# Optimization experiments

Hardware: AMD Instinct MI355X
Metric: run time of the kernel (lower is better)

## Reference

```python
import jax, jax.numpy as jnp
import numpy as np

B, T, I, H, O = 64, 32, 512, 256, 512
NPRE = 25  # range(1, 26) in the source


def _lstm(xg, whh, mask, reverse):
    """xg: [B,T,4H] precomputed input-gate activations; mask: [T] bool.
    Masked steps keep the carry unchanged (carry starts at zeros, and the
    invalid region is always a contiguous run at the start of the scan
    direction, so this exactly reproduces running the LSTM on the valid
    sub-sequence only)."""
    nb = xg.shape[0]
    nh = whh.shape[1]

    def step(carry, inp):
        h, c = carry
        g, m = inp
        z = g + h @ whh.T  # [B,4H]
        i, f, gg, o = jnp.split(z, 4, axis=-1)  # torch gate order i,f,g,o
        c2 = jax.nn.sigmoid(f) * c + jax.nn.sigmoid(i) * jnp.tanh(gg)
        h2 = jax.nn.sigmoid(o) * jnp.tanh(c2)
        h2 = jnp.where(m, h2, h)
        c2 = jnp.where(m, c2, c)
        return (h2, c2), h2

    init = (jnp.zeros((nb, nh), xg.dtype), jnp.zeros((nb, nh), xg.dtype))
    xs = (jnp.swapaxes(xg, 0, 1), mask[:, None, None])  # time-major
    _, hs = jax.lax.scan(step, init, xs, reverse=reverse)
    return jnp.swapaxes(hs, 0, 1)  # [B,T,H]


def _bilstm(x, mask, wif, whf, bf, wib, whb, bb):
    xgf = jnp.einsum('bti,gi->btg', x, wif) + bf
    xgb = jnp.einsum('bti,gi->btg', x, wib) + bb
    hf = _lstm(xgf, whf, mask, reverse=False)
    hb = _lstm(xgb, whb, mask, reverse=True)
    return jnp.concatenate([hf, hb], axis=-1)  # [B,T,2H]


def setup_inputs() -> dict:
    key = jax.random.key(0)
    ks = jax.random.split(key, 16)
    s = 1.0 / np.sqrt(H)
    u = lambda k, shp: jax.random.uniform(k, shp, jnp.float32, -s, s)
    return {
        'x': jax.random.normal(ks[0], (B, T, I), jnp.float32),
        'w_ih_f': u(ks[1], (4 * H, I)), 'w_hh_f': u(ks[2], (4 * H, H)), 'b_f': u(ks[3], (4 * H,)),
        'w_ih_b': u(ks[4], (4 * H, I)), 'w_hh_b': u(ks[5], (4 * H, H)), 'b_b': u(ks[6], (4 * H,)),
        'w2_ih_f': u(ks[7], (4 * H, H)), 'w2_hh_f': u(ks[8], (4 * H, H)), 'b2_f': u(ks[9], (4 * H,)),
        'w2_ih_b': u(ks[10], (4 * H, H)), 'w2_hh_b': u(ks[11], (4 * H, H)), 'b2_b': u(ks[12], (4 * H,)),
        'wl': u(ks[13], (O, 4 * H)), 'bl': u(ks[14], (O,)),
    }


def reference(x, w_ih_f, w_hh_f, b_f, w_ih_b, w_hh_b, b_b,
              w2_ih_f, w2_hh_f, b2_f, w2_ih_b, w2_hh_b, b2_b, wl, bl):
    t_idx = jnp.arange(T)
    lens = jnp.arange(1, NPRE + 1)
    pre_masks = t_idx[None, :] < lens[:, None]   # [25,T]: input[:, :i]
    suf_masks = t_idx[None, :] >= lens[:, None]  # [25,T]: input[:, j:]

    run = jax.vmap(lambda m: _bilstm(x, m, w_ih_f, w_hh_f, b_f, w_ih_b, w_hh_b, b_b))
    pre = run(pre_masks)  # [25,B,T,2H]
    suf = run(suf_masks)  # [25,B,T,2H]

    neg = jnp.finfo(x.dtype).min
    prefix_pool = jnp.where(pre_masks[:, None, :, None], pre, neg).max(axis=2)  # [25,B,2H]
    suffix_pool = jnp.where(suf_masks[:, None, :, None], suf, neg).max(axis=2)  # [25,B,2H]

    full = jnp.ones((T,), bool)
    r2 = _bilstm(x[:, :, :H], full, w2_ih_f, w2_hh_f, b2_f, w2_ih_b, w2_hh_b, b2_b)
    r3 = _bilstm(x[:, :, H:], full, w2_ih_f, w2_hh_f, b2_f, w2_ih_b, w2_hh_b, b2_b)
    r4 = jnp.concatenate([r2, r3], axis=-1)  # [B,T,4H]
    output = r4 @ wl.T + bl  # [B,T,O]
    return output, prefix_pool, suffix_pool
```

## Files before the change

### kernel.cpp

```cpp
#include <hip/hip_runtime.h>
#include <math.h>

#define BB 64
#define TT 32
#define II 512
#define HH 256
#define ZN 1024
#define OO 512
#define NPRE 25

typedef unsigned short u16;
typedef unsigned long long u64;
typedef short bfrag __attribute__((ext_vector_type(8)));
typedef _Float16 hfrag __attribute__((ext_vector_type(8)));
typedef float f32x4 __attribute__((ext_vector_type(4)));

__device__ __forceinline__ float sigm_(float x) { return 1.f / (1.f + __expf(-x)); }
__device__ __forceinline__ float tanh_(float x) { return 1.f - 2.f / (__expf(2.f * x) + 1.f); }

__device__ __forceinline__ u16 f2bf(float x) {
    union { float f; unsigned u; } v; v.f = x;
    unsigned r = v.u + 0x7fffu + ((v.u >> 16) & 1u);
    return (u16)(r >> 16);
}
__device__ __forceinline__ float bf2f(u16 b) {
    union { unsigned u; float f; } v; v.u = ((unsigned)b) << 16; return v.f;
}
__device__ __forceinline__ u16 f2h_bits(float x) {
    union { _Float16 h; u16 u; } v; v.h = (_Float16)x; return v.u;
}

__global__ __launch_bounds__(256) void prep_frag(
    const float* __restrict__ src, int ld,
    u16* __restrict__ hi, u16* __restrict__ lo)
{
    const int T  = gridDim.x >> 1;
    const int e2 = blockIdx.x * 256 + threadIdx.x;
    const int kt = blockIdx.y;
    const int i = e2 & 7, l = (e2 >> 3) & 63, t = e2 >> 9;
    const int d = t * 16 + (l & 15);
    const int k = kt * 32 + ((l >> 4) << 3) + i;
    const float v = src[(size_t)d * ld + k];
    const u16 h = f2bf(v);
    const size_t o = (size_t)kt * ((size_t)T * 512) + e2;
    hi[o] = h;
    lo[o] = f2bf(v - bf2f(h));
}

__global__ __launch_bounds__(256) void prep_w4h(
    const float* __restrict__ s0, const float* __restrict__ s1,
    const float* __restrict__ s2, const float* __restrict__ s3,
    _Float16* __restrict__ dst)
{
    const int z = blockIdx.z;
    const float* src = (z == 0) ? s0 : (z == 1) ? s1 : (z == 2) ? s2 : s3;
    const int e2 = blockIdx.x * 256 + threadIdx.x;
    const int kt = blockIdx.y;
    const int i = e2 & 7, l = (e2 >> 3) & 63, t = e2 >> 9;
    const int d = t * 16 + (l & 15);
    const int k = kt * 32 + ((l >> 4) << 3) + i;
    dst[(size_t)z * 262144 + (size_t)kt * 32768 + e2] =
        (_Float16)src[(size_t)d * HH + k];
}

__global__ __launch_bounds__(256) void prep_w2(
    const float* __restrict__ s0, const float* __restrict__ s1,
    u16* __restrict__ hi, u16* __restrict__ lo)
{
    const int z = blockIdx.z;
    const float* src = z ? s1 : s0;
    const int e2 = blockIdx.x * 256 + threadIdx.x;
    const int kt = blockIdx.y;
    const int i = e2 & 7, l = (e2 >> 3) & 63, t = e2 >> 9;
    const int d = t * 16 + (l & 15);
    const int k = kt * 32 + ((l >> 4) << 3) + i;
    const float v = src[(size_t)d * HH + k];
    const u16 h = f2bf(v);
    const size_t o = (size_t)z * 262144 + (size_t)kt * 32768 + e2;
    hi[o] = h;
    lo[o] = f2bf(v - bf2f(h));
}

__global__ __launch_bounds__(256) void prep_w16(
    const float* __restrict__ s0, const float* __restrict__ s1,
    u16* __restrict__ hi, u16* __restrict__ lo)
{
    const int z = blockIdx.z;
    const float* src = z ? s1 : s0;
    const int e2 = blockIdx.x * 256 + threadIdx.x;
    const int kt = blockIdx.y;
    const int i = e2 & 7, l = (e2 >> 3) & 63, t = e2 >> 9;
    const int d = t * 16 + (l & 15);
    const int k = kt * 32 + ((l >> 4) << 3) + i;
    const float v = src[(size_t)d * II + k];
    const u16 h = f2bf(v);
    const size_t o = (size_t)z * 524288 + (size_t)kt * 32768 + e2;
    hi[o] = h;
    lo[o] = f2bf(v - bf2f(h));
}

__global__ __launch_bounds__(256) void prep_x_tmajor(
    const float* __restrict__ x, u16* __restrict__ hi, u16* __restrict__ lo)
{
    const int e2 = blockIdx.x * 256 + threadIdx.x;
    const int kt = blockIdx.y;
    const int i = e2 & 7, l = (e2 >> 3) & 63, mt = e2 >> 9;
    const int d = mt * 16 + (l & 15);
    const int t = d >> 6, row = d & 63;
    const int k = kt * 32 + ((l >> 4) << 3) + i;
    const float v = x[((size_t)row * TT + t) * II + k];
    const u16 h = f2bf(v);
    const size_t o = (size_t)kt * 65536 + e2;
    hi[o] = h;
    lo[o] = f2bf(v - bf2f(h));
}

__global__ __launch_bounds__(256) void gemm_mfma(
    const u16* __restrict__ Ahi, const u16* __restrict__ Alo, const int MT, const int kt0,
    const u16* __restrict__ Bhi, const u16* __restrict__ Blo, const int NT,
    const float* __restrict__ bias,
    float* __restrict__ C, const int ldc, const int KT)
{
    const int tid = threadIdx.x;
    const int w = tid >> 6, l = tid & 63;
    const int mt0 = blockIdx.y * 4;
    const int nt0 = blockIdx.x * 16 + w * 4;

    f32x4 acc[4][4];
    #pragma unroll
    for (int a = 0; a < 4; ++a)
        #pragma unroll
        for (int b = 0; b < 4; ++b) acc[a][b] = (f32x4){0.f, 0.f, 0.f, 0.f};

    bfrag ah0[4], al0[4], bh0[4], bl0[4];
    bfrag ah1[4], al1[4], bh1[4], bl1[4];

#define LOADF(AH, AL, BH, BL, KIDX) do {                                          \
    const int kk_ = (KIDX);                                                      \
    _Pragma("unroll") for (int mt = 0; mt < 4; ++mt) {                            \
        const size_t oa = (((size_t)(kt0 + kk_) * MT + mt0 + mt) * 64 + l) * 8;   \
        AH[mt] = *(const bfrag*)(Ahi + oa); AL[mt] = *(const bfrag*)(Alo + oa); } \
    _Pragma("unroll") for (int j = 0; j < 4; ++j) {                               \
        const size_t ob = (((size_t)kk_ * NT + nt0 + j) * 64 + l) * 8;            \
        BH[j] = *(const bfrag*)(Bhi + ob); BL[j] = *(const bfrag*)(Blo + ob); }   \
} while (0)

#define MFMAS(AH, AL, BH, BL) do {                                                \
    _Pragma("unroll") for (int mt = 0; mt < 4; ++mt)                              \
    _Pragma("unroll") for (int j = 0; j < 4; ++j) {                               \
        acc[mt][j] = __builtin_amdgcn_mfma_f32_16x16x32_bf16(AH[mt], BH[j], acc[mt][j], 0, 0, 0); \
        acc[mt][j] = __builtin_amdgcn_mfma_f32_16x16x32_bf16(AH[mt], BL[j], acc[mt][j], 0, 0, 0); \
        acc[mt][j] = __builtin_amdgcn_mfma_f32_16x16x32_bf16(AL[mt], BH[j], acc[mt][j], 0, 0, 0); } \
} while (0)

    LOADF(ah0, al0, bh0, bl0, 0);
    for (int kt = 0; kt < KT; kt += 2) {
        LOADF(ah1, al1, bh1, bl1, kt + 1);
        MFMAS(ah0, al0, bh0, bl0);
        if (kt + 2 < KT) LOADF(ah0, al0, bh0, bl0, kt + 2);
        MFMAS(ah1, al1, bh1, bl1);
    }

    const int rsub = (l >> 4) << 2;
    #pragma unroll
    for (int j = 0; j < 4; ++j) {
        const int col = (nt0 + j) * 16 + (l & 15);
        const float bv = bias[col];
        #pragma unroll
        for (int mt = 0; mt < 4; ++mt)
            #pragma unroll
            for (int reg = 0; reg < 4; ++reg)
                C[(size_t)((mt0 + mt) * 16 + rsub + reg) * ldc + col] = acc[mt][j][reg] + bv;
    }
#undef LOADF
#undef MFMAS
}

__global__ __launch_bounds__(256) void gemm_xg(
    const u16* __restrict__ Ahi, const u16* __restrict__ Alo, const int kt0h,
    const u16* __restrict__ Bhi0, const u16* __restrict__ Blo0, const size_t bstride,
    const float* __restrict__ bias_even, const float* __restrict__ bias_odd,
    float* __restrict__ out0, const int KT)
{
    const int MT = 128, NT = 64;
    const int z = blockIdx.z;
    const int kt0 = (z >> 1) * kt0h;
    const u16* Bhi = Bhi0 + (size_t)(z & 1) * bstride;
    const u16* Blo = Blo0 + (size_t)(z & 1) * bstride;
    const float* bias = (z & 1) ? bias_odd : bias_even;
    float* out = out0 + (size_t)z * ((size_t)BB * TT * ZN);

    const int tid = threadIdx.x;
    const int w = tid >> 6, l = tid & 63;
    const int t = blockIdx.y;
    const int mt0 = t * 4;
    const int nt0 = blockIdx.x * 16 + w * 4;

    f32x4 acc[4][4];
    #pragma unroll
    for (int a = 0; a < 4; ++a)
        #pragma unroll
        for (int b = 0; b < 4; ++b) acc[a][b] = (f32x4){0.f, 0.f, 0.f, 0.f};

    bfrag ah0[4], al0[4], bh0[4], bl0[4];
    bfrag ah1[4], al1[4], bh1[4], bl1[4];

#define LOADF(AH, AL, BH, BL, KIDX) do {                                          \
    const int kk_ = (KIDX);                                                      \
    _Pragma("unroll") for (int mt = 0; mt < 4; ++mt) {                            \
        const size_t oa = (((size_t)(kt0 + kk_) * MT + mt0 + mt) * 64 + l) * 8;   \
        AH[mt] = *(const bfrag*)(Ahi + oa); AL[mt] = *(const bfrag*)(Alo + oa); } \
    _Pragma("unroll") for (int j = 0; j < 4; ++j) {                               \
        const size_t ob = (((size_t)kk_ * NT + nt0 + j) * 64 + l) * 8;            \
        BH[j] = *(const bfrag*)(Bhi + ob); BL[j] = *(const bfrag*)(Blo + ob); }   \
} while (0)

#define MFMAS(AH, AL, BH, BL) do {                                                \
    _Pragma("unroll") for (int mt = 0; mt < 4; ++mt)                              \
    _Pragma("unroll") for (int j = 0; j < 4; ++j) {                               \
        acc[mt][j] = __builtin_amdgcn_mfma_f32_16x16x32_bf16(AH[mt], BH[j], acc[mt][j], 0, 0, 0); \
        acc[mt][j] = __builtin_amdgcn_mfma_f32_16x16x32_bf16(AH[mt], BL[j], acc[mt][j], 0, 0, 0); \
        acc[mt][j] = __builtin_amdgcn_mfma_f32_16x16x32_bf16(AL[mt], BH[j], acc[mt][j], 0, 0, 0); } \
} while (0)

    LOADF(ah0, al0, bh0, bl0, 0);
    for (int kt = 0; kt < KT; kt += 2) {
        LOADF(ah1, al1, bh1, bl1, kt + 1);
        MFMAS(ah0, al0, bh0, bl0);
        if (kt + 2 < KT) LOADF(ah0, al0, bh0, bl0, kt + 2);
        MFMAS(ah1, al1, bh1, bl1);
    }
#undef LOADF
#undef MFMAS

    const int cl = l & 15;
    #pragma unroll
    for (int j = 0; j < 4; ++j) {
        const float bv = bias[(nt0 + j) * 16 + cl];
        #pragma unroll
        for (int mt = 0; mt < 4; ++mt) {
            f32x4 o = acc[mt][j];
            o[0] += bv; o[1] += bv; o[2] += bv; o[3] += bv;
            *(f32x4*)(out + ((((size_t)t * 64 + nt0 + j) * 4 + mt) * 64 + l) * 4) = o;
        }
    }
}

__global__ __launch_bounds__(256, 2) void lstm_runs_k(
    const int s0, const int s1,
    const float* __restrict__ xgfP, const float* __restrict__ xgbP,
    const float* __restrict__ xg2P,
    const _Float16* __restrict__ W16,
    u64* __restrict__ hU, unsigned* __restrict__ bar,
    float* __restrict__ c_st, float* __restrict__ mx_st,
    float* __restrict__ out_pre, float* __restrict__ out_suf,
    u16* __restrict__ r4Ah, u16* __restrict__ r4Al)
{
    __shared__ u16 hh[2][16384];

    const int wg  = blockIdx.x;
    const int rid = wg % 56;
    const int q   = wg / 56;
    const int tid = threadIdx.x;
    const int w   = tid >> 6;
    const int l   = tid & 63;
    const bool coop = (s1 - s0) > 1;

    const float* xg; int wmat, t0, dt, ns, mode, len = 0, part = 0;
    if (rid == 0)      { mode = 0; ns = 32; t0 = 0;  dt = 1;  xg = xgfP; wmat = 0; }
    else if (rid == 1) { mode = 1; ns = 32; t0 = 31; dt = -1; xg = xgbP; wmat = 1; }
    else if (rid < 27) { mode = 2; len = rid - 1;  ns = len;      t0 = len - 1; dt = -1; xg = xgbP; wmat = 1; }
    else if (rid < 52) { mode = 3; len = rid - 26; ns = 32 - len; t0 = len;     dt = 1;  xg = xgfP; wmat = 0; }
    else { mode = 4; part = rid - 52; ns = 32;
           xg = xg2P + (size_t)part * ((size_t)BB * TT * ZN);
           wmat = 2 + (part & 1); if (part & 1) { t0 = 31; dt = -1; } else { t0 = 0; dt = 1; } }

    if (!coop && s0 >= ns) return;

    hfrag WH[8][4];
    {
        const _Float16* WHp = W16 + (size_t)wmat * 262144;
        #pragma unroll
        for (int kt = 0; kt < 8; ++kt)
            #pragma unroll
            for (int g = 0; g < 4; ++g) {
                const size_t ob = (((size_t)kt * 64 + g * 16 + q * 4 + w) * 64 + l) * 8;
                WH[kt][g] = *(const hfrag*)(WHp + ob);
            }
    }

    const int cl = l & 15, rsub = (l >> 4) << 2;
    const int hc = q * 64 + w * 16 + cl;
    const int kt2 = hc >> 5, i2 = hc & 7, lhi = (hc >> 3) & 3;
    const size_t stBase = ((size_t)wg * 256 + tid) * 16;
    const int kk4 = part * 256 + hc;
    const int ktp4 = kk4 >> 5, lph = ((kk4 >> 3) & 3) * 16, ip = kk4 & 7;
    const int rw = tid >> 6, rcl = tid & 15, rsw = ((tid >> 4) & 3) << 2;

    float c[4][4], mx[4][4];
    if (s0 == 0) {
        #pragma unroll
        for (int a = 0; a < 4; ++a)
            #pragma unroll
            for (int b = 0; b < 4; ++b) { c[a][b] = 0.f; mx[a][b] = -3.4e38f; }
    } else {
        #pragma unroll
        for (int mt = 0; mt < 4; ++mt) {
            const f32x4 cv = *(const f32x4*)(c_st  + stBase + mt * 4);
            const f32x4 mv = *(const f32x4*)(mx_st + stBase + mt * 4);
            #pragma unroll
            for (int r = 0; r < 4; ++r) { c[mt][r] = cv[r]; mx[mt][r] = mv[r]; }
        }
    }

    for (int s = s0; s < s1; ++s) {
        if (s >= ns) break;
        const int t = t0 + dt * s;
        const int sp  = s & 1;
        const int spn = sp ^ 1;

        f32x4 acc[4][4];
        #pragma unroll
        for (int a = 0; a < 4; ++a)
            #pragma unroll
            for (int b = 0; b < 4; ++b) acc[a][b] = (f32x4){0.f, 0.f, 0.f, 0.f};

        if (s > 0) {
            if (coop && tid == 0) {
                unsigned v;
                do {
                    v = __hip_atomic_load(&bar[rid * 32], __ATOMIC_RELAXED,
                                          __HIP_MEMORY_SCOPE_AGENT);
                    if (v < (unsigned)(4 * s)) __builtin_amdgcn_s_sleep(2);
                } while (v < (unsigned)(4 * s));
                (void)__hip_atomic_load(&bar[rid * 32], __ATOMIC_ACQUIRE,
                                        __HIP_MEMORY_SCOPE_AGENT);
            }
            __syncthreads();

            const u64* srcU = hU + ((size_t)sp * 56 + rid) * 4096;
            #pragma unroll
            for (int qp = 0; qp < 4; ++qp) {
                if (coop && qp == q) continue;
                const int col = qp * 64 + rw * 16 + rcl;
                const int ktc = col >> 5, lqc = (col >> 3) & 3, i2c = col & 7;
                u64 vals[4];
                #pragma unroll
                for (int mt = 0; mt < 4; ++mt)
                    vals[mt] = __hip_atomic_load(srcU + (qp * 4 + mt) * 256 + tid,
                                                 __ATOMIC_RELAXED, __HIP_MEMORY_SCOPE_AGENT);
                #pragma unroll
                for (int mt = 0; mt < 4; ++mt) {
                    #pragma unroll
                    for (int rr = 0; rr < 4; ++rr) {
                        const int fi = ((ktc * 4 + mt) * 64 + rsw + rr + 16 * lqc) * 8 + i2c;
                        hh[sp][fi] = (u16)(vals[mt] >> (16 * rr));
                    }
                }
            }
            __syncthreads();

            #pragma unroll
            for (int kt = 0; kt < 8; ++kt) {
                hfrag ah[4];
                #pragma unroll
                for (int mt = 0; mt < 4; ++mt)
                    ah[mt] = *(const hfrag*)&hh[sp][((kt * 4 + mt) * 64 + l) * 8];
                #pragma unroll
                for (int mt = 0; mt < 4; ++mt)
                    #pragma unroll
                    for (int g = 0; g < 4; ++g)
                        acc[mt][g] = __builtin_amdgcn_mfma_f32_16x16x32_f16(
                            ah[mt], WH[kt][g], acc[mt][g], 0, 0, 0);
            }
        }

        u64* dstU = hU + ((size_t)spn * 56 + rid) * 4096 + q * 1024 + tid;

        #pragma unroll
        for (int mt = 0; mt < 4; ++mt) {
            f32x4 xv[4];
            #pragma unroll
            for (int g = 0; g < 4; ++g)
                xv[g] = *(const f32x4*)(xg + ((((size_t)t * 64 + g * 16 + q * 4 + w) * 4 + mt) * 64 + l) * 4);
            u64 pk = 0;
            #pragma unroll
            for (int reg = 0; reg < 4; ++reg) {
                const int row = mt * 16 + rsub + reg;
                const float zi = acc[mt][0][reg] + xv[0][reg];
                const float zf = acc[mt][1][reg] + xv[1][reg];
                const float zg = acc[mt][2][reg] + xv[2][reg];
                const float zo = acc[mt][3][reg] + xv[3][reg];
                const float c2 = sigm_(zf) * c[mt][reg] + sigm_(zi) * tanh_(zg);
                const float h2 = sigm_(zo) * tanh_(c2);
                c[mt][reg] = c2;
                const float m2 = fmaxf(mx[mt][reg], h2);
                mx[mt][reg] = m2;

                const u16 uhf = f2h_bits(h2);
                pk |= (u64)uhf << (16 * reg);

                hh[spn][((kt2 * 4 + mt) * 64 + rsub + reg + 16 * lhi) * 8 + i2] = uhf;

                if (mode == 0) {
                    if (t <= 24)
                        __builtin_nontemporal_store(m2,
                            out_pre + ((size_t)t * BB + row) * (2 * HH) + hc);
                } else if (mode == 1) {
                    if (t >= 1 && t <= 25)
                        __builtin_nontemporal_store(m2,
                            out_suf + ((size_t)(t - 1) * BB + row) * (2 * HH) + HH + hc);
                } else if (mode == 2) {
                    if (s == ns - 1)
                        __builtin_nontemporal_store(m2,
                            out_pre + ((size_t)(len - 1) * BB + row) * (2 * HH) + HH + hc);
                } else if (mode == 3) {
                    if (s == ns - 1)
                        __builtin_nontemporal_store(m2,
                            out_suf + ((size_t)(len - 1) * BB + row) * (2 * HH) + hc);
                } else {
                    const int d = row * 32 + t;
                    const size_t idx = (((size_t)ktp4 * 128 + (d >> 4)) * 64
                                        + lph + (d & 15)) * 8 + ip;
                    const u16 ubh = f2bf(h2);
                    __builtin_nontemporal_store(ubh, r4Ah + idx);
                    __builtin_nontemporal_store(f2bf(h2 - bf2f(ubh)), r4Al + idx);
                }
            }
            __hip_atomic_store(dstU + mt * 256, pk,
                               __ATOMIC_RELAXED, __HIP_MEMORY_SCOPE_AGENT);
        }

        if (coop && s + 1 < ns) {
            __syncthreads();
            if (tid == 0)
                __hip_atomic_fetch_add(&bar[rid * 32], 1u, __ATOMIC_RELEASE,
                                       __HIP_MEMORY_SCOPE_AGENT);
        }
    }

    if (!coop && s1 < TT) {
        #pragma unroll
        for (int mt = 0; mt < 4; ++mt) {
            f32x4 cv, mv;
            #pragma unroll
            for (int r = 0; r < 4; ++r) { cv[r] = c[mt][r]; mv[r] = mx[mt][r]; }
            *(f32x4*)(c_st  + stBase + mt * 4) = cv;
            *(f32x4*)(mx_st + stBase + mt * 4) = mv;
        }
    }
}

extern "C" void kernel_launch(void* const* d_in, const int* in_sizes, int n_in,
                              void* d_out, int out_size, void* d_ws, size_t ws_size,
                              hipStream_t stream)
{
    const float* x    = (const float*)d_in[0];
    const float* wif  = (const float*)d_in[1];
    const float* whf  = (const float*)d_in[2];
    const float* bf   = (const float*)d_in[3];
    const float* wib  = (const float*)d_in[4];
    const float* whb  = (const float*)d_in[5];
    const float* bb   = (const float*)d_in[6];
    const float* w2if = (const float*)d_in[7];
    const float* w2hf = (const float*)d_in[8];
    const float* b2f  = (const float*)d_in[9];
    const float* w2ib = (const float*)d_in[10];
    const float* w2hb = (const float*)d_in[11];
    const float* b2b  = (const float*)d_in[12];
    const float* wl   = (const float*)d_in[13];
    const float* bl   = (const float*)d_in[14];

    const size_t XG = (size_t)BB * TT * ZN;
    float* xgfP  = (float*)d_ws;
    float* xgbP  = xgfP + XG;
    float* xg2P  = xgbP + XG;
    float* c_st  = xg2P + 4 * XG;
    float* mx_st = c_st + (size_t)224 * 256 * 16;

    u16* p = (u16*)(mx_st + (size_t)224 * 256 * 16);
    u16* WB2h  = p; p += (size_t)2 * 262144;
    u16* WB2l  = p; p += (size_t)2 * 262144;
    u16* WB16h = p; p += (size_t)2 * 524288;
    u16* WB16l = p; p += (size_t)2 * 524288;
    u16* wlBh  = p; p += (size_t)524288;
    u16* wlBl  = p; p += (size_t)524288;
    u16* xAh   = p; p += (size_t)2048 * 512;
    u16* xAl   = p; p += (size_t)2048 * 512;
    u16* r4Ah  = p; p += (size_t)2048 * 1024;
    u16* r4Al  = p; p += (size_t)2048 * 1024;
    _Float16* W16 = (_Float16*)p; p += (size_t)4 * 262144;
    u64* hU = (u64*)(((uintptr_t)p + 15) & ~(uintptr_t)15);
    unsigned* bar = (unsigned*)(hU + (size_t)2 * 56 * 4096);

    float* outp    = (float*)d_out;
    float* out_pre = outp + (size_t)BB * TT * OO;
    float* out_suf = out_pre + (size_t)NPRE * BB * (2 * HH);

    hipMemsetAsync(bar, 0, (size_t)56 * 32 * sizeof(unsigned), stream);

    prep_w4h<<<dim3(128, 8, 4),  256, 0, stream>>>(whf, whb, w2hf, w2hb, W16);
    prep_w2 <<<dim3(128, 8, 2),  256, 0, stream>>>(w2if, w2ib, WB2h, WB2l);
    prep_w16<<<dim3(128, 16, 2), 256, 0, stream>>>(wif, wib, WB16h, WB16l);
    prep_frag<<<dim3(64, 32),    256, 0, stream>>>(wl, ZN, wlBh, wlBl);
    prep_x_tmajor<<<dim3(256, 16), 256, 0, stream>>>(x, xAh, xAl);

    gemm_xg<<<dim3(4, 32, 2), 256, 0, stream>>>(xAh, xAl, 0, WB16h, WB16l, 524288,
                                                bf, bb, xgfP, 16);
    gemm_xg<<<dim3(4, 32, 4), 256, 0, stream>>>(xAh, xAl, 8, WB2h, WB2l, 262144,
                                                b2f, b2b, xg2P, 8);

    {
        int cs0 = 0, cs1 = TT;
        const float* a_xgf = xgfP; const float* a_xgb = xgbP; const float* a_xg2 = xg2P;
        const _Float16* a_w16 = W16;
        u64* a_hu = hU; unsigned* a_bar = bar;
        float* a_cst = c_st; float* a_mx = mx_st;
        float* a_pre = out_pre; float* a_suf = out_suf;
        u16* a_r4h = r4Ah; u16* a_r4l = r4Al;
        void* cargs[] = { (void*)&cs0, (void*)&cs1,
                          (void*)&a_xgf, (void*)&a_xgb, (void*)&a_xg2,
                          (void*)&a_w16,
                          (void*)&a_hu, (void*)&a_bar,
                          (void*)&a_cst, (void*)&a_mx,
                          (void*)&a_pre, (void*)&a_suf,
                          (void*)&a_r4h, (void*)&a_r4l };
        hipError_t ce = hipLaunchCooperativeKernel((const void*)lstm_runs_k,
                                                   dim3(224), dim3(256), cargs, 0, stream);
        if (ce != hipSuccess) {
            for (int s = 0; s < TT; ++s)
                lstm_runs_k<<<dim3(224), dim3(256), 0, stream>>>(s, s + 1,
                    xgfP, xgbP, xg2P, W16, hU, bar, c_st, mx_st,
                    out_pre, out_suf, r4Ah, r4Al);
        }
    }

    gemm_mfma<<<dim3(2, 32), 256, 0, stream>>>(r4Ah, r4Al, 128, 0, wlBh, wlBl, 32, bl, outp, OO, 32);
}
```

Measured before the change: 638.7 us.

## Split LSTM runs by batch rows into independent 1024-thread workgroups

```diff
diff --git a/kernel.cpp b/kernel.cpp
--- a/kernel.cpp
+++ b/kernel.cpp
@@ -10,7 +10,6 @@
 #define NPRE 25
 
 typedef unsigned short u16;
-typedef unsigned long long u64;
 typedef short bfrag __attribute__((ext_vector_type(8)));
 typedef _Float16 hfrag __attribute__((ext_vector_type(8)));
 typedef float f32x4 __attribute__((ext_vector_type(4)));
@@ -246,25 +245,21 @@
     }
 }
 
-__global__ __launch_bounds__(256, 2) void lstm_runs_k(
-    const int s0, const int s1,
+__global__ __launch_bounds__(1024, 1) void lstm_wg(
     const float* __restrict__ xgfP, const float* __restrict__ xgbP,
     const float* __restrict__ xg2P,
     const _Float16* __restrict__ W16,
-    u64* __restrict__ hU, unsigned* __restrict__ bar,
-    float* __restrict__ c_st, float* __restrict__ mx_st,
     float* __restrict__ out_pre, float* __restrict__ out_suf,
     u16* __restrict__ r4Ah, u16* __restrict__ r4Al)
 {
-    __shared__ u16 hh[2][16384];
+    __shared__ u16 hh[2][4096];
 
     const int wg  = blockIdx.x;
-    const int rid = wg % 56;
-    const int q   = wg / 56;
+    const int rid = wg >> 2;
+    const int r   = wg & 3;
     const int tid = threadIdx.x;
     const int w   = tid >> 6;
     const int l   = tid & 63;
-    const bool coop = (s1 - s0) > 1;
 
     const float* xg; int wmat, t0, dt, ns, mode, len = 0, part = 0;
     if (rid == 0)      { mode = 0; ns = 32; t0 = 0;  dt = 1;  xg = xgfP; wmat = 0; }
@@ -275,8 +270,6 @@
            xg = xg2P + (size_t)part * ((size_t)BB * TT * ZN);
            wmat = 2 + (part & 1); if (part & 1) { t0 = 31; dt = -1; } else { t0 = 0; dt = 1; } }
 
-    if (!coop && s0 >= ns) return;
-
     hfrag WH[8][4];
     {
         const _Float16* WHp = W16 + (size_t)wmat * 262144;
@@ -284,170 +277,92 @@
         for (int kt = 0; kt < 8; ++kt)
             #pragma unroll
             for (int g = 0; g < 4; ++g) {
-                const size_t ob = (((size_t)kt * 64 + g * 16 + q * 4 + w) * 64 + l) * 8;
+                const size_t ob = (((size_t)kt * 64 + g * 16 + w) * 64 + l) * 8;
                 WH[kt][g] = *(const hfrag*)(WHp + ob);
             }
     }
 
-    const int cl = l & 15, rsub = (l >> 4) << 2;
-    const int hc = q * 64 + w * 16 + cl;
-    const int kt2 = hc >> 5, i2 = hc & 7, lhi = (hc >> 3) & 3;
-    const size_t stBase = ((size_t)wg * 256 + tid) * 16;
+    const int cl  = l & 15;
+    const int lr4 = (l >> 4) << 2;
+    const int hc  = w * 16 + cl;
+    const int kt2 = hc >> 5, i2 = hc & 7, lq = (hc >> 3) & 3;
     const int kk4 = part * 256 + hc;
     const int ktp4 = kk4 >> 5, lph = ((kk4 >> 3) & 3) * 16, ip = kk4 & 7;
-    const int rw = tid >> 6, rcl = tid & 15, rsw = ((tid >> 4) & 3) << 2;
-
-    float c[4][4], mx[4][4];
-    if (s0 == 0) {
-        #pragma unroll
-        for (int a = 0; a < 4; ++a)
-            #pragma unroll
-            for (int b = 0; b < 4; ++b) { c[a][b] = 0.f; mx[a][b] = -3.4e38f; }
-    } else {
-        #pragma unroll
-        for (int mt = 0; mt < 4; ++mt) {
-            const f32x4 cv = *(const f32x4*)(c_st  + stBase + mt * 4);
-            const f32x4 mv = *(const f32x4*)(mx_st + stBase + mt * 4);
-            #pragma unroll
-            for (int r = 0; r < 4; ++r) { c[mt][r] = cv[r]; mx[mt][r] = mv[r]; }
-        }
-    }
-
-    for (int s = s0; s < s1; ++s) {
-        if (s >= ns) break;
+
+    float c[4], mx[4];
+    #pragma unroll
+    for (int e = 0; e < 4; ++e) { c[e] = 0.f; mx[e] = -3.4e38f; }
+
+    for (int s = 0; s < ns; ++s) {
         const int t = t0 + dt * s;
         const int sp  = s & 1;
         const int spn = sp ^ 1;
 
-        f32x4 acc[4][4];
-        #pragma unroll
-        for (int a = 0; a < 4; ++a)
-            #pragma unroll
-            for (int b = 0; b < 4; ++b) acc[a][b] = (f32x4){0.f, 0.f, 0.f, 0.f};
+        f32x4 xv[4];
+        #pragma unroll
+        for (int g = 0; g < 4; ++g)
+            xv[g] = *(const f32x4*)(xg +
+                ((((size_t)t * 64 + g * 16 + w) * 4 + r) * 64 + l) * 4);
+
+        f32x4 acc[4];
+        #pragma unroll
+        for (int g = 0; g < 4; ++g) acc[g] = (f32x4){0.f, 0.f, 0.f, 0.f};
 
         if (s > 0) {
-            if (coop && tid == 0) {
-                unsigned v;
-                do {
-                    v = __hip_atomic_load(&bar[rid * 32], __ATOMIC_RELAXED,
-                                          __HIP_MEMORY_SCOPE_AGENT);
-                    if (v < (unsigned)(4 * s)) __builtin_amdgcn_s_sleep(2);
-                } while (v < (unsigned)(4 * s));
-                (void)__hip_atomic_load(&bar[rid * 32], __ATOMIC_ACQUIRE,
-                                        __HIP_MEMORY_SCOPE_AGENT);
-            }
-            __syncthreads();
-
-            const u64* srcU = hU + ((size_t)sp * 56 + rid) * 4096;
-            #pragma unroll
-            for (int qp = 0; qp < 4; ++qp) {
-                if (coop && qp == q) continue;
-                const int col = qp * 64 + rw * 16 + rcl;
-                const int ktc = col >> 5, lqc = (col >> 3) & 3, i2c = col & 7;
-                u64 vals[4];
-                #pragma unroll
-                for (int mt = 0; mt < 4; ++mt)
-                    vals[mt] = __hip_atomic_load(srcU + (qp * 4 + mt) * 256 + tid,
-                                                 __ATOMIC_RELAXED, __HIP_MEMORY_SCOPE_AGENT);
-                #pragma unroll
-                for (int mt = 0; mt < 4; ++mt) {
-                    #pragma unroll
-                    for (int rr = 0; rr < 4; ++rr) {
-                        const int fi = ((ktc * 4 + mt) * 64 + rsw + rr + 16 * lqc) * 8 + i2c;
-                        hh[sp][fi] = (u16)(vals[mt] >> (16 * rr));
-                    }
-                }
-            }
-            __syncthreads();
-
             #pragma unroll
             for (int kt = 0; kt < 8; ++kt) {
-                hfrag ah[4];
+                const hfrag ah = *(const hfrag*)&hh[sp][(kt * 64 + l) * 8];
                 #pragma unroll
-                for (int mt = 0; mt < 4; ++mt)
-                    ah[mt] = *(const hfrag*)&hh[sp][((kt * 4 + mt) * 64 + l) * 8];
-                #pragma unroll
-                for (int mt = 0; mt < 4; ++mt)
-                    #pragma unroll
-                    for (int g = 0; g < 4; ++g)
-                        acc[mt][g] = __builtin_amdgcn_mfma_f32_16x16x32_f16(
-                            ah[mt], WH[kt][g], acc[mt][g], 0, 0, 0);
+                for (int g = 0; g < 4; ++g)
+                    acc[g] = __builtin_amdgcn_mfma_f32_16x16x32_f16(
+                        ah, WH[kt][g], acc[g], 0, 0, 0);
             }
         }
 
-        u64* dstU = hU + ((size_t)spn * 56 + rid) * 4096 + q * 1024 + tid;
-
-        #pragma unroll
-        for (int mt = 0; mt < 4; ++mt) {
-            f32x4 xv[4];
-            #pragma unroll
-            for (int g = 0; g < 4; ++g)
-                xv[g] = *(const f32x4*)(xg + ((((size_t)t * 64 + g * 16 + q * 4 + w) * 4 + mt) * 64 + l) * 4);
-            u64 pk = 0;
-            #pragma unroll
-            for (int reg = 0; reg < 4; ++reg) {
-                const int row = mt * 16 + rsub + reg;
-                const float zi = acc[mt][0][reg] + xv[0][reg];
-                const float zf = acc[mt][1][reg] + xv[1][reg];
-                const float zg = acc[mt][2][reg] + xv[2][reg];
-                const float zo = acc[mt][3][reg] + xv[3][reg];
-                const float c2 = sigm_(zf) * c[mt][reg] + sigm_(zi) * tanh_(zg);
-                const float h2 = sigm_(zo) * tanh_(c2);
-                c[mt][reg] = c2;
-                const float m2 = fmaxf(mx[mt][reg], h2);
-                mx[mt][reg] = m2;
-
-                const u16 uhf = f2h_bits(h2);
-                pk |= (u64)uhf << (16 * reg);
-
-                hh[spn][((kt2 * 4 + mt) * 64 + rsub + reg + 16 * lhi) * 8 + i2] = uhf;
-
-                if (mode == 0) {
-                    if (t <= 24)
-                        __builtin_nontemporal_store(m2,
-                            out_pre + ((size_t)t * BB + row) * (2 * HH) + hc);
-                } else if (mode == 1) {
-                    if (t >= 1 && t <= 25)
-                        __builtin_nontemporal_store(m2,
-                            out_suf + ((size_t)(t - 1) * BB + row) * (2 * HH) + HH + hc);
-                } else if (mode == 2) {
-                    if (s == ns - 1)
-                        __builtin_nontemporal_store(m2,
-                            out_pre + ((size_t)(len - 1) * BB + row) * (2 * HH) + HH + hc);
-                } else if (mode == 3) {
-                    if (s == ns - 1)
-                        __builtin_nontemporal_store(m2,
-                            out_suf + ((size_t)(len - 1) * BB + row) * (2 * HH) + hc);
-                } else {
-                    const int d = row * 32 + t;
-                    const size_t idx = (((size_t)ktp4 * 128 + (d >> 4)) * 64
-                                        + lph + (d & 15)) * 8 + ip;
-                    const u16 ubh = f2bf(h2);
-                    __builtin_nontemporal_store(ubh, r4Ah + idx);
-                    __builtin_nontemporal_store(f2bf(h2 - bf2f(ubh)), r4Al + idx);
-                }
+        #pragma unroll
+        for (int reg = 0; reg < 4; ++reg) {
+            const int rowl = lr4 + reg;
+            const int row  = r * 16 + rowl;
+            const float zi = acc[0][reg] + xv[0][reg];
+            const float zf = acc[1][reg] + xv[1][reg];
+            const float zg = acc[2][reg] + xv[2][reg];
+            const float zo = acc[3][reg] + xv[3][reg];
+            const float c2 = sigm_(zf) * c[reg] + sigm_(zi) * tanh_(zg);
+            const float h2 = sigm_(zo) * tanh_(c2);
+            c[reg] = c2;
+            const float m2 = fmaxf(mx[reg], h2);
+            mx[reg] = m2;
+
+            const u16 uhf = f2h_bits(h2);
+            hh[spn][(kt2 * 64 + rowl + 16 * lq) * 8 + i2] = uhf;
+
+            if (mode == 0) {
+                if (t <= 24)
+                    __builtin_nontemporal_store(m2,
+                        out_pre + ((size_t)t * BB + row) * (2 * HH) + hc);
+            } else if (mode == 1) {
+                if (t >= 1 && t <= 25)
+                    __builtin_nontemporal_store(m2,
+                        out_suf + ((size_t)(t - 1) * BB + row) * (2 * HH) + HH + hc);
+            } else if (mode == 2) {
+                if (s == ns - 1)
+                    __builtin_nontemporal_store(m2,
+                        out_pre + ((size_t)(len - 1) * BB + row) * (2 * HH) + HH + hc);
+            } else if (mode == 3) {
+                if (s == ns - 1)
+                    __builtin_nontemporal_store(m2,
+                        out_suf + ((size_t)(len - 1) * BB + row) * (2 * HH) + hc);
+            } else {
+                const int d = row * 32 + t;
+                const size_t idx = (((size_t)ktp4 * 128 + (d >> 4)) * 64
+                                    + lph + (d & 15)) * 8 + ip;
+                const u16 ubh = f2bf(h2);
+                __builtin_nontemporal_store(ubh, r4Ah + idx);
+                __builtin_nontemporal_store(f2bf(h2 - bf2f(ubh)), r4Al + idx);
             }
-            __hip_atomic_store(dstU + mt * 256, pk,
-                               __ATOMIC_RELAXED, __HIP_MEMORY_SCOPE_AGENT);
         }
 
-        if (coop && s + 1 < ns) {
-            __syncthreads();
-            if (tid == 0)
-                __hip_atomic_fetch_add(&bar[rid * 32], 1u, __ATOMIC_RELEASE,
-                                       __HIP_MEMORY_SCOPE_AGENT);
-        }
-    }
-
-    if (!coop && s1 < TT) {
-        #pragma unroll
-        for (int mt = 0; mt < 4; ++mt) {
-            f32x4 cv, mv;
-            #pragma unroll
-            for (int r = 0; r < 4; ++r) { cv[r] = c[mt][r]; mv[r] = mx[mt][r]; }
-            *(f32x4*)(c_st  + stBase + mt * 4) = cv;
-            *(f32x4*)(mx_st + stBase + mt * 4) = mv;
-        }
+        __syncthreads();
     }
 }
 
@@ -475,10 +390,8 @@
     float* xgfP  = (float*)d_ws;
     float* xgbP  = xgfP + XG;
     float* xg2P  = xgbP + XG;
-    float* c_st  = xg2P + 4 * XG;
-    float* mx_st = c_st + (size_t)224 * 256 * 16;
-
-    u16* p = (u16*)(mx_st + (size_t)224 * 256 * 16);
+
+    u16* p = (u16*)(xg2P + 4 * XG);
     u16* WB2h  = p; p += (size_t)2 * 262144;
     u16* WB2l  = p; p += (size_t)2 * 262144;
     u16* WB16h = p; p += (size_t)2 * 524288;
@@ -489,15 +402,11 @@
     u16* xAl   = p; p += (size_t)2048 * 512;
     u16* r4Ah  = p; p += (size_t)2048 * 1024;
     u16* r4Al  = p; p += (size_t)2048 * 1024;
-    _Float16* W16 = (_Float16*)p; p += (size_t)4 * 262144;
-    u64* hU = (u64*)(((uintptr_t)p + 15) & ~(uintptr_t)15);
-    unsigned* bar = (unsigned*)(hU + (size_t)2 * 56 * 4096);
+    _Float16* W16 = (_Float16*)p;
 
     float* outp    = (float*)d_out;
     float* out_pre = outp + (size_t)BB * TT * OO;
     float* out_suf = out_pre + (size_t)NPRE * BB * (2 * HH);
-
-    hipMemsetAsync(bar, 0, (size_t)56 * 32 * sizeof(unsigned), stream);
 
     prep_w4h<<<dim3(128, 8, 4),  256, 0, stream>>>(whf, whb, w2hf, w2hb, W16);
     prep_w2 <<<dim3(128, 8, 2),  256, 0, stream>>>(w2if, w2ib, WB2h, WB2l);
@@ -510,30 +419,8 @@
     gemm_xg<<<dim3(4, 32, 4), 256, 0, stream>>>(xAh, xAl, 8, WB2h, WB2l, 262144,
                                                 b2f, b2b, xg2P, 8);
 
-    {
-        int cs0 = 0, cs1 = TT;
-        const float* a_xgf = xgfP; const float* a_xgb = xgbP; const float* a_xg2 = xg2P;
-        const _Float16* a_w16 = W16;
-        u64* a_hu = hU; unsigned* a_bar = bar;
-        float* a_cst = c_st; float* a_mx = mx_st;
-        float* a_pre = out_pre; float* a_suf = out_suf;
-        u16* a_r4h = r4Ah; u16* a_r4l = r4Al;
-        void* cargs[] = { (void*)&cs0, (void*)&cs1,
-                          (void*)&a_xgf, (void*)&a_xgb, (void*)&a_xg2,
-                          (void*)&a_w16,
-                          (void*)&a_hu, (void*)&a_bar,
-                          (void*)&a_cst, (void*)&a_mx,
-                          (void*)&a_pre, (void*)&a_suf,
-                          (void*)&a_r4h, (void*)&a_r4l };
-        hipError_t ce = hipLaunchCooperativeKernel((const void*)lstm_runs_k,
-                                                   dim3(224), dim3(256), cargs, 0, stream);
-        if (ce != hipSuccess) {
-            for (int s = 0; s < TT; ++s)
-                lstm_runs_k<<<dim3(224), dim3(256), 0, stream>>>(s, s + 1,
-                    xgfP, xgbP, xg2P, W16, hU, bar, c_st, mx_st,
-                    out_pre, out_suf, r4Ah, r4Al);
-        }
-    }
+    lstm_wg<<<dim3(224), dim3(1024), 0, stream>>>(xgfP, xgbP, xg2P, W16,
+                                                  out_pre, out_suf, r4Ah, r4Al);
 
     gemm_mfma<<<dim3(2, 32), 256, 0, stream>>>(r4Ah, r4Al, 128, 0, wlBh, wlBl, 32, bl, outp, OO, 32);
 }
```

After: 523.3 us. 18.1% less time.
